# Optimization experiments

Measured on AMD Instinct MI355X. Metric: run time of the kernel, lower is better.

The kernel has to match this reference:

```python
import jax, jax.numpy as jnp
import numpy as np

STATE_DIM = 256
LATENT_DIM = 64
HIDDEN = 64
NUM_EMB = 2048
BATCH = 32768


def setup_inputs() -> dict:
    key = jax.random.key(0)
    ks = jax.random.split(key, 10)
    s = lambda *sh: 1.0 / np.sqrt(sh[0])
    return {
        "x": jax.random.normal(ks[0], (BATCH, STATE_DIM), dtype=jnp.float32),
        # encoder: Linear(state_dim, 64) -> ReLU -> Linear(64, latent_dim)
        "enc_w1": jax.random.uniform(ks[1], (STATE_DIM, HIDDEN), jnp.float32, -s(STATE_DIM), s(STATE_DIM)),
        "enc_b1": jax.random.uniform(ks[2], (HIDDEN,), jnp.float32, -s(STATE_DIM), s(STATE_DIM)),
        "enc_w2": jax.random.uniform(ks[3], (HIDDEN, LATENT_DIM), jnp.float32, -s(HIDDEN), s(HIDDEN)),
        "enc_b2": jax.random.uniform(ks[4], (LATENT_DIM,), jnp.float32, -s(HIDDEN), s(HIDDEN)),
        # codebook
        "emb": jax.random.normal(ks[5], (NUM_EMB, LATENT_DIM), dtype=jnp.float32),
        # decoder: Linear(latent_dim, 64) -> ReLU -> Linear(64, state_dim)
        "dec_w1": jax.random.uniform(ks[6], (LATENT_DIM, HIDDEN), jnp.float32, -s(LATENT_DIM), s(LATENT_DIM)),
        "dec_b1": jax.random.uniform(ks[7], (HIDDEN,), jnp.float32, -s(LATENT_DIM), s(LATENT_DIM)),
        "dec_w2": jax.random.uniform(ks[8], (HIDDEN, STATE_DIM), jnp.float32, -s(HIDDEN), s(HIDDEN)),
        "dec_b2": jax.random.uniform(ks[9], (STATE_DIM,), jnp.float32, -s(HIDDEN), s(HIDDEN)),
    }


def reference(x, enc_w1, enc_b1, enc_w2, enc_b2, emb, dec_w1, dec_b1, dec_w2, dec_b2):
    # encoder MLP: z_e [B, latent]
    h = jax.nn.relu(x @ enc_w1 + enc_b1)
    z_e = h @ enc_w2 + enc_b2
    # squared euclidean distances to codebook, expanded form: [B, K]
    # ||z - e||^2 = ||z||^2 - 2 z.e + ||e||^2  (same argmin as broadcast form)
    d = (jnp.sum(z_e * z_e, axis=1, keepdims=True)
         - 2.0 * (z_e @ emb.T)
         + jnp.sum(emb * emb, axis=1)[None, :])
    z_q_idx = jnp.argmin(d, axis=1)           # [B]
    z_q = emb[z_q_idx]                        # [B, latent]
    # decoder MLP
    hd = jax.nn.relu(z_q @ dec_w1 + dec_b1)
    x_recon = hd @ dec_w2 + dec_b2
    return (x_recon, z_e, z_q)
```

## Files before the change

### kernel.cpp

```cpp
#include <hip/hip_runtime.h>

#define BATCH   32768
#define SD      256
#define LD      64
#define HDIM    64
#define NEMB    2048
#define REFINE_THR_Q 5e-4f

typedef short  short8 __attribute__((ext_vector_type(8)));
typedef float  f32x4  __attribute__((ext_vector_type(4)));

__device__ __forceinline__ unsigned short f2bf(float f) {
    unsigned int u = __float_as_uint(f);
    u = (u + 0x7FFFu + ((u >> 16) & 1u)) >> 16;
    return (unsigned short)u;
}
__device__ __forceinline__ float bf2f(unsigned short h) {
    return __uint_as_float(((unsigned int)h) << 16);
}

__global__ __launch_bounds__(256) void k0_prep(const float* __restrict__ emb,
                                               float* __restrict__ e2q,
                                               unsigned short* __restrict__ eh,
                                               unsigned short* __restrict__ el,
                                               int* __restrict__ count) {
    int k = blockIdx.x * 256 + threadIdx.x;
    if (k == 0) *count = 0;
    const float* er = emb + (size_t)k * LD;
    unsigned short hrow[LD], lrow[LD];
    float s = 0.f;
#pragma unroll
    for (int q = 0; q < LD; ++q) {
        float v = er[q];
        s += v * v;
        unsigned short h = f2bf(v);
        hrow[q] = h;
        lrow[q] = f2bf(v - bf2f(h));
    }
    e2q[k] = -0.5f * s;
    short8* dh = (short8*)(eh + (size_t)k * LD);
    short8* dl = (short8*)(el + (size_t)k * LD);
#pragma unroll
    for (int q = 0; q < 8; ++q) {
        dh[q] = *(short8*)&hrow[q * 8];
        dl[q] = *(short8*)&lrow[q * 8];
    }
}

__global__ __launch_bounds__(256) void k0b_wsplit(const float* __restrict__ w1,
                                                  const float* __restrict__ w2,
                                                  unsigned short* __restrict__ w1h,
                                                  unsigned short* __restrict__ w1l,
                                                  unsigned short* __restrict__ w2h,
                                                  unsigned short* __restrict__ w2l) {
    int b = blockIdx.x;
    int t = threadIdx.x;
    if (b < 16) {
        int e = b * 256 + t;
        int j = e >> 6, k = e & 63;
        float v = w1[k * HDIM + j];
        unsigned short h = f2bf(v);
        w1h[e] = h; w1l[e] = f2bf(v - bf2f(h));
    } else {
        int e = (b - 16) * 256 + t;
        int j = e >> 6, k = e & 63;
        float v = w2[k * SD + j];
        unsigned short h = f2bf(v);
        w2h[e] = h; w2l[e] = f2bf(v - bf2f(h));
    }
}

__global__ __launch_bounds__(512, 4) void k_enc(const float* __restrict__ x,
                                                const float* __restrict__ w1,
                                                const float* __restrict__ b1,
                                                const float* __restrict__ w2,
                                                const float* __restrict__ b2,
                                                float* __restrict__ zOut,
                                                unsigned short* __restrict__ zh,
                                                unsigned short* __restrict__ zl) {
    __shared__ float smem[20480];
    float* w1s = smem;
    float* xs  = smem + 16384;
    int tid = threadIdx.x;
    {
        const float4* src = (const float4*)w1;
        float4* dst = (float4*)w1s;
#pragma unroll
        for (int t = 0; t < 8; ++t) dst[tid + 512 * t] = src[tid + 512 * t];
    }
    int r0 = blockIdx.x * 64;
    int sr = tid >> 3;
    int sq = tid & 7;
    const float* xrow = x + (size_t)(r0 + sr) * SD + sq * 4;
    *(float4*)&xs[sr * 32 + sq * 4] = *(const float4*)xrow;
    __syncthreads();

    int lane = tid & 63;
    int w = tid >> 6;
    float acc[8];
#pragma unroll
    for (int r = 0; r < 8; ++r) acc[r] = 0.f;

    for (int c = 0; c < 8; ++c) {
        float4 nv;
        if (c < 7) nv = *(const float4*)(xrow + (c + 1) * 32);
        const float* xb = &xs[(c & 1) * 2048 + (w * 8) * 32];
        int kb = c * 32;
#pragma unroll
        for (int i0 = 0; i0 < 32; i0 += 8) {
            float wf[8];
#pragma unroll
            for (int jj = 0; jj < 8; ++jj) wf[jj] = w1s[(kb + i0 + jj) * HDIM + lane];
#pragma unroll
            for (int r = 0; r < 8; ++r) {
                const float* xr = xb + r * 32 + i0;
                float4 xa = *(const float4*)xr;
                float4 xc = *(const float4*)(xr + 4);
                acc[r] += xa.x * wf[0] + xa.y * wf[1] + xa.z * wf[2] + xa.w * wf[3]
                        + xc.x * wf[4] + xc.y * wf[5] + xc.z * wf[6] + xc.w * wf[7];
            }
        }
        __syncthreads();
        if (c < 7) *(float4*)&xs[((c + 1) & 1) * 2048 + sr * 32 + sq * 4] = nv;
        __syncthreads();
    }

    float* hs  = smem;
    float* w2s = smem + 4096;
    float bb1 = b1[lane];
#pragma unroll
    for (int r = 0; r < 8; ++r)
        hs[(w * 8 + r) * 64 + lane] = fmaxf(acc[r] + bb1, 0.f);
    {
        const float4* src = (const float4*)w2;
        float4* dst = (float4*)w2s;
        dst[tid] = src[tid];
        dst[tid + 512] = src[tid + 512];
    }
    __syncthreads();

    const float* hb = &hs[(w * 8) * 64];
    float ac2[8];
#pragma unroll
    for (int r = 0; r < 8; ++r) ac2[r] = 0.f;

    for (int j0 = 0; j0 < HDIM; j0 += 8) {
        float wf[8];
#pragma unroll
        for (int jj = 0; jj < 8; ++jj) wf[jj] = w2s[(j0 + jj) * LD + lane];
#pragma unroll
        for (int r = 0; r < 8; ++r) {
            const float* hr = hb + r * 64 + j0;
            float4 ha = *(const float4*)hr;
            float4 hc = *(const float4*)(hr + 4);
            ac2[r] += ha.x * wf[0] + ha.y * wf[1] + ha.z * wf[2] + ha.w * wf[3]
                    + hc.x * wf[4] + hc.y * wf[5] + hc.z * wf[6] + hc.w * wf[7];
        }
    }
    float bb2 = b2[lane];
#pragma unroll
    for (int r = 0; r < 8; ++r) {
        float z = ac2[r] + bb2;
        size_t o = (size_t)(r0 + w * 8 + r) * LD + lane;
        zOut[o] = z;
        unsigned short h = f2bf(z);
        zh[o] = h;
        zl[o] = f2bf(z - bf2f(h));
    }
}

#define K2_LOAD(P, t) do {                                                  \
    const unsigned short* ph_ = ehp + (size_t)(t) * 16 * LD;                \
    const unsigned short* pl_ = elp + (size_t)(t) * 16 * LD;                \
    P##a0 = *(const short8*)(ph_);                                          \
    P##a1 = *(const short8*)(ph_ + 32);                                     \
    P##a2 = *(const short8*)(pl_);                                          \
    P##a3 = *(const short8*)(pl_ + 32);                                     \
    P##e2 = *(const f32x4*)(e2q + cbase + (t) * 16 + hi * 4);               \
} while (0)

#define K2_COMP(P, t) do {                                                  \
    f32x4 acc_[4];                                                          \
    _Pragma("unroll")                                                       \
    for (int g = 0; g < 4; ++g) {                                           \
        f32x4 c_;                                                           \
        c_ = __builtin_amdgcn_mfma_f32_16x16x32_bf16(P##a0, bh[g][0], P##e2, 0, 0, 0); \
        c_ = __builtin_amdgcn_mfma_f32_16x16x32_bf16(P##a1, bh[g][1], c_, 0, 0, 0);    \
        c_ = __builtin_amdgcn_mfma_f32_16x16x32_bf16(P##a2, bh[g][0], c_, 0, 0, 0);    \
        c_ = __builtin_amdgcn_mfma_f32_16x16x32_bf16(P##a3, bh[g][1], c_, 0, 0, 0);    \
        c_ = __builtin_amdgcn_mfma_f32_16x16x32_bf16(P##a0, bl[g][0], c_, 0, 0, 0);    \
        c_ = __builtin_amdgcn_mfma_f32_16x16x32_bf16(P##a1, bl[g][1], c_, 0, 0, 0);    \
        acc_[g] = c_;                                                       \
    }                                                                       \
    _Pragma("unroll")                                                       \
    for (int g = 0; g < 4; ++g) {                                           \
        float m_ = fmaxf(fmaxf(acc_[g][0], acc_[g][1]),                     \
                         fmaxf(acc_[g][2], acc_[g][3]));                    \
        bool win_ = (m_ > bb[g]);                                           \
        qv[g] = win_ ? acc_[g] : qv[g];                                     \
        tt[g] = win_ ? (t) : tt[g];                                         \
        b2v[g] = fmaxf(b2v[g], fminf(bb[g], m_));                           \
        bb[g] = fmaxf(bb[g], m_);                                           \
    }                                                                       \
} while (0)

__global__ __launch_bounds__(256, 2) void k2_mfma(const unsigned short* __restrict__ zh,
                                                  const unsigned short* __restrict__ zl,
                                                  const unsigned short* __restrict__ eh,
                                                  const unsigned short* __restrict__ el,
                                                  const float* __restrict__ e2q,
                                                  int* __restrict__ idx,
                                                  int* __restrict__ list,
                                                  int* __restrict__ count) {
    int tid  = threadIdx.x;
    int lane = tid & 63;
    int w    = tid >> 6;
    int rb   = blockIdx.x * 64;
    int lo   = lane & 15;
    int hi   = lane >> 4;

    short8 bh[4][2], bl[4][2];
#pragma unroll
    for (int g = 0; g < 4; ++g) {
        size_t zo = (size_t)(rb + g * 16 + lo) * LD + hi * 8;
        bh[g][0] = *(const short8*)(zh + zo);
        bh[g][1] = *(const short8*)(zh + zo + 32);
        bl[g][0] = *(const short8*)(zl + zo);
        bl[g][1] = *(const short8*)(zl + zo + 32);
    }

    float bb[4], b2v[4];
    f32x4 qv[4];
    int   tt[4];
#pragma unroll
    for (int g = 0; g < 4; ++g) {
        bb[g] = -3.0e38f; b2v[g] = -3.0e38f; tt[g] = 0;
        qv[g][0] = qv[g][1] = qv[g][2] = qv[g][3] = -3.0e38f;
    }

    const int cbase = w * (NEMB / 4);
    const unsigned short* ehp = eh + (size_t)(cbase + lo) * LD + hi * 8;
    const unsigned short* elp = el + (size_t)(cbase + lo) * LD + hi * 8;

    short8 Aa0, Aa1, Aa2, Aa3; f32x4 Ae2;
    short8 Ba0, Ba1, Ba2, Ba3; f32x4 Be2;
    short8 Ca0, Ca1, Ca2, Ca3; f32x4 Ce2;

    K2_LOAD(A, 0);
    K2_LOAD(B, 1);
    K2_LOAD(C, 2);

    for (int tb = 0; tb < 27; tb += 3) {
        K2_COMP(A, tb);     K2_LOAD(A, tb + 3);
        K2_COMP(B, tb + 1); K2_LOAD(B, tb + 4);
        K2_COMP(C, tb + 2); K2_LOAD(C, tb + 5);
    }
    K2_COMP(A, 27); K2_LOAD(A, 30);
    K2_COMP(B, 28); K2_LOAD(B, 31);
    K2_COMP(C, 29);
    K2_COMP(A, 30);
    K2_COMP(B, 31);

    float ss[4];
    int   ii[4];
#pragma unroll
    for (int g = 0; g < 4; ++g) {
        float s0 = qv[g][0], s1 = qv[g][1], s2 = qv[g][2], s3 = qv[g][3];
        float M01 = fmaxf(s0, s1), L01 = fminf(s0, s1);
        float M23 = fmaxf(s2, s3), L23 = fminf(s2, s3);
        int   d01 = (s1 > s0) ? 1 : 0;
        int   d23 = (s3 > s2) ? 3 : 2;
        bool  cp  = (M23 > M01);
        float within2 = fmaxf(fminf(M01, M23), cp ? L23 : L01);
        int   dd  = cp ? d23 : d01;
        ii[g] = cbase + tt[g] * 16 + hi * 4 + dd;
        ss[g] = fmaxf(b2v[g], within2);
    }

#pragma unroll
    for (int off = 16; off <= 32; off <<= 1) {
#pragma unroll
        for (int g = 0; g < 4; ++g) {
            float ob = __shfl_xor(bb[g], off);
            float os = __shfl_xor(ss[g], off);
            int   oi = __shfl_xor(ii[g], off);
            ss[g] = fmaxf(fmaxf(fminf(bb[g], ob), os), ss[g]);
            ii[g] = (ob > bb[g]) ? oi : ii[g];
            bb[g] = fmaxf(bb[g], ob);
        }
    }

    __shared__ float Lb[4][64];
    __shared__ float Ls[4][64];
    __shared__ int   Li[4][64];
    if (lane < 16) {
#pragma unroll
        for (int g = 0; g < 4; ++g) {
            Lb[w][g * 16 + lane] = bb[g];
            Ls[w][g * 16 + lane] = ss[g];
            Li[w][g * 16 + lane] = ii[g];
        }
    }
    __syncthreads();

    if (tid < 64) {
        float B = Lb[0][tid], S = Ls[0][tid];
        int   I = Li[0][tid];
#pragma unroll
        for (int w2 = 1; w2 < 4; ++w2) {
            float ob = Lb[w2][tid], os = Ls[w2][tid];
            int   oi = Li[w2][tid];
            S = fmaxf(fmaxf(fminf(B, ob), os), S);
            I = (ob > B) ? oi : I;
            B = fmaxf(B, ob);
        }
        idx[rb + tid] = I;
        if (B - S < REFINE_THR_Q) {
            int p = atomicAdd(count, 1);
            list[p] = rb + tid;
        }
    }
}

__global__ __launch_bounds__(256) void k3_refine(const float* __restrict__ z,
                                                 const float* __restrict__ emb,
                                                 const int* __restrict__ count,
                                                 const int* __restrict__ list,
                                                 int* __restrict__ idx) {
    __shared__ double sv[256];
    __shared__ int    sx[256];
    int tid = threadIdx.x;
    int n = *count;
    for (int g = blockIdx.x; g < n; g += gridDim.x) {
        int row = list[g];
        const float4* zr4 = (const float4*)(z + (size_t)row * LD);
        float4 zv[16];
#pragma unroll
        for (int q = 0; q < 16; ++q) zv[q] = zr4[q];

        double best = 1.0e300;
        int bi = NEMB;
#pragma unroll 2
        for (int c = 0; c < 8; ++c) {
            int k = tid * 8 + c;
            const float4* er = (const float4*)(emb + (size_t)k * LD);
            double d0 = 0.0, d1 = 0.0, d2 = 0.0, d3 = 0.0;
#pragma unroll
            for (int q = 0; q < 16; ++q) {
                float4 e4 = er[q];
                double tx = (double)zv[q].x - (double)e4.x;
                double ty = (double)zv[q].y - (double)e4.y;
                double tz = (double)zv[q].z - (double)e4.z;
                double tw = (double)zv[q].w - (double)e4.w;
                d0 += tx * tx; d1 += ty * ty; d2 += tz * tz; d3 += tw * tw;
            }
            double d = (d0 + d1) + (d2 + d3);
            if (d < best) { best = d; bi = k; }
        }
        sv[tid] = best; sx[tid] = bi;
        __syncthreads();
        for (int s = 128; s > 0; s >>= 1) {
            if (tid < s) {
                if (sv[tid + s] < sv[tid] ||
                    (sv[tid + s] == sv[tid] && sx[tid + s] < sx[tid])) {
                    sv[tid] = sv[tid + s]; sx[tid] = sx[tid + s];
                }
            }
            __syncthreads();
        }
        if (tid == 0) idx[row] = sx[0];
        __syncthreads();
    }
}

__global__ __launch_bounds__(256, 2) void k_dec(const int* __restrict__ idx,
                                                const float* __restrict__ emb,
                                                const unsigned short* __restrict__ w1h,
                                                const unsigned short* __restrict__ w1l,
                                                const float* __restrict__ b1,
                                                const unsigned short* __restrict__ w2h,
                                                const unsigned short* __restrict__ w2l,
                                                const float* __restrict__ b2,
                                                float* __restrict__ xrec,
                                                float* __restrict__ zq) {
    __shared__ float hds[4][16 * 68];
    int tid  = threadIdx.x;
    int lane = tid & 63;
    int w    = tid >> 6;
    int lo   = lane & 15;
    int hi   = lane >> 4;
    int rb   = blockIdx.x * 64 + w * 16;
    int row  = rb + lo;
    int ix   = idx[row];

    short8 zah[2], zal[2];
    {
        const float* er  = emb + (size_t)ix * LD + hi * 8;
        float* zqr = zq + (size_t)row * LD + hi * 8;
#pragma unroll
        for (int kt = 0; kt < 2; ++kt) {
            float4 a = *(const float4*)(er + kt * 32);
            float4 b = *(const float4*)(er + kt * 32 + 4);
            *(float4*)(zqr + kt * 32) = a;
            *(float4*)(zqr + kt * 32 + 4) = b;
            float v[8] = {a.x, a.y, a.z, a.w, b.x, b.y, b.z, b.w};
            unsigned short hh[8], ll[8];
#pragma unroll
            for (int q = 0; q < 8; ++q) {
                unsigned short hb = f2bf(v[q]);
                hh[q] = hb;
                ll[q] = f2bf(v[q] - bf2f(hb));
            }
            zah[kt] = *(short8*)hh;
            zal[kt] = *(short8*)ll;
        }
    }

#pragma unroll
    for (int jt = 0; jt < 4; ++jt) {
        float bj = b1[jt * 16 + lo];
        f32x4 c = {bj, bj, bj, bj};
#pragma unroll
        for (int kt = 0; kt < 2; ++kt) {
            short8 bh8 = *(const short8*)(w1h + (jt * 16 + lo) * LD + kt * 32 + hi * 8);
            short8 bl8 = *(const short8*)(w1l + (jt * 16 + lo) * LD + kt * 32 + hi * 8);
            c = __builtin_amdgcn_mfma_f32_16x16x32_bf16(zah[kt], bh8, c, 0, 0, 0);
            c = __builtin_amdgcn_mfma_f32_16x16x32_bf16(zah[kt], bl8, c, 0, 0, 0);
            c = __builtin_amdgcn_mfma_f32_16x16x32_bf16(zal[kt], bh8, c, 0, 0, 0);
        }
#pragma unroll
        for (int r = 0; r < 4; ++r)
            hds[w][(hi * 4 + r) * 68 + jt * 16 + lo] = fmaxf(c[r], 0.f);
    }
    __syncthreads();

    short8 hah[2], hal[2];
#pragma unroll
    for (int kt = 0; kt < 2; ++kt) {
        float4 a = *(const float4*)&hds[w][lo * 68 + kt * 32 + hi * 8];
        float4 b = *(const float4*)&hds[w][lo * 68 + kt * 32 + hi * 8 + 4];
        float v[8] = {a.x, a.y, a.z, a.w, b.x, b.y, b.z, b.w};
        unsigned short hh[8], ll[8];
#pragma unroll
        for (int q = 0; q < 8; ++q) {
            unsigned short hb = f2bf(v[q]);
            hh[q] = hb;
            ll[q] = f2bf(v[q] - bf2f(hb));
        }
        hah[kt] = *(short8*)hh;
        hal[kt] = *(short8*)ll;
    }

    for (int jt = 0; jt < 16; ++jt) {
        float bj = b2[jt * 16 + lo];
        f32x4 c = {bj, bj, bj, bj};
#pragma unroll
        for (int kt = 0; kt < 2; ++kt) {
            short8 bh8 = *(const short8*)(w2h + (jt * 16 + lo) * LD + kt * 32 + hi * 8);
            short8 bl8 = *(const short8*)(w2l + (jt * 16 + lo) * LD + kt * 32 + hi * 8);
            c = __builtin_amdgcn_mfma_f32_16x16x32_bf16(hah[kt], bh8, c, 0, 0, 0);
            c = __builtin_amdgcn_mfma_f32_16x16x32_bf16(hah[kt], bl8, c, 0, 0, 0);
            c = __builtin_amdgcn_mfma_f32_16x16x32_bf16(hal[kt], bh8, c, 0, 0, 0);
        }
#pragma unroll
        for (int r = 0; r < 4; ++r)
            xrec[(size_t)(rb + hi * 4 + r) * SD + jt * 16 + lo] = c[r];
    }
}

extern "C" void kernel_launch(void* const* d_in, const int* in_sizes, int n_in,
                              void* d_out, int out_size, void* d_ws, size_t ws_size,
                              hipStream_t stream) {
    const float* x   = (const float*)d_in[0];
    const float* ew1 = (const float*)d_in[1];
    const float* eb1 = (const float*)d_in[2];
    const float* ew2 = (const float*)d_in[3];
    const float* eb2 = (const float*)d_in[4];
    const float* emb = (const float*)d_in[5];
    const float* dw1 = (const float*)d_in[6];
    const float* db1 = (const float*)d_in[7];
    const float* dw2 = (const float*)d_in[8];
    const float* db2 = (const float*)d_in[9];

    float* out  = (float*)d_out;
    float* xrec = out;
    float* zE   = out + (size_t)BATCH * SD;
    float* zQ   = zE + (size_t)BATCH * LD;

    char* xb = (char*)xrec;
    unsigned short* zh  = (unsigned short*)xb;
    unsigned short* zl  = (unsigned short*)(xb + (4u << 20));
    unsigned short* eh  = (unsigned short*)(xb + (8u << 20));
    unsigned short* el  = (unsigned short*)(xb + (8u << 20) + (NEMB * LD * 2));
    float*          e2q = (float*)(xb + (9u << 20));

    char* ws = (char*)d_ws;
    int*  count = (int*)ws;
    int*  idxA  = (int*)(ws + 16384);
    int*  list  = (int*)(ws + 147456);
    unsigned short* w1h = (unsigned short*)(ws + 278528);
    unsigned short* w1l = (unsigned short*)(ws + 286720);
    unsigned short* w2h = (unsigned short*)(ws + 294912);
    unsigned short* w2l = (unsigned short*)(ws + 327680);

    hipLaunchKernelGGL(k0_prep,    dim3(NEMB / 256), dim3(256), 0, stream, emb, e2q, eh, el, count);
    hipLaunchKernelGGL(k0b_wsplit, dim3(80),         dim3(256), 0, stream, dw1, dw2, w1h, w1l, w2h, w2l);
    hipLaunchKernelGGL(k_enc,      dim3(BATCH / 64), dim3(512), 0, stream, x, ew1, eb1, ew2, eb2, zE, zh, zl);
    hipLaunchKernelGGL(k2_mfma,    dim3(BATCH / 64), dim3(256), 0, stream, zh, zl, eh, el, e2q, idxA, list, count);
    hipLaunchKernelGGL(k3_refine,  dim3(128),        dim3(256), 0, stream, zE, emb, count, list, idxA);
    hipLaunchKernelGGL(k_dec,      dim3(BATCH / 64), dim3(256), 0, stream, idxA, emb, w1h, w1l, db1, w2h, w2l, db2, xrec, zQ);
}
```

Measured before the change: 129.9 us.

## Rework encoder GEMMs as 8x8 register-tiled split-K with shared-memory reduction

The encoder kernel now stages the whole 64x256 x tile transposed in LDS. Each thread computes an 8x8 output tile with outer-product FMAs, and each of the 8 waves handles a K-slice. Partial sums are combined by a tree reduction through shared memory, and the same scheme is applied to the second layer. The goal is more FMAs per LDS load. The cost is extra syncs, a serial reduction tail done by one wave, larger LDS use (128KB) and launch bounds lowered to 2 blocks per SM.

Result: no change. 132.3 us (+1.9%).

```diff
diff --git a/kernel.cpp b/kernel.cpp
--- a/kernel.cpp
+++ b/kernel.cpp
@@ -70,7 +70,46 @@
     }
 }
 
-__global__ __launch_bounds__(512, 4) void k_enc(const float* __restrict__ x,
+__device__ __forceinline__ void wr_slice(float* red, int s, float (&a)[8][8],
+                                         int rg, int cg) {
+#pragma unroll
+    for (int cc = 0; cc < 8; ++cc) {
+        float4 v0 = {a[0][cc], a[1][cc], a[2][cc], a[3][cc]};
+        float4 v1 = {a[4][cc], a[5][cc], a[6][cc], a[7][cc]};
+        float* p = red + s * 4096 + (cg * 8 + cc) * 64 + rg * 8;
+        *(float4*)p = v0;
+        *(float4*)(p + 4) = v1;
+    }
+}
+__device__ __forceinline__ void add_slice(float* red, int s, float (&a)[8][8],
+                                          int rg, int cg) {
+#pragma unroll
+    for (int cc = 0; cc < 8; ++cc) {
+        const float* p = red + s * 4096 + (cg * 8 + cc) * 64 + rg * 8;
+        float4 v0 = *(const float4*)p;
+        float4 v1 = *(const float4*)(p + 4);
+        a[0][cc] += v0.x; a[1][cc] += v0.y; a[2][cc] += v0.z; a[3][cc] += v0.w;
+        a[4][cc] += v1.x; a[5][cc] += v1.y; a[6][cc] += v1.z; a[7][cc] += v1.w;
+    }
+}
+__device__ __forceinline__ void enc_merge(float* red, float (&a)[8][8],
+                                          int w, int rg, int cg) {
+    if (w & 1) wr_slice(red, w >> 1, a, rg, cg);
+    __syncthreads();
+    if (!(w & 1)) add_slice(red, w >> 1, a, rg, cg);
+    __syncthreads();
+    if (w == 2) wr_slice(red, 0, a, rg, cg);
+    if (w == 6) wr_slice(red, 1, a, rg, cg);
+    __syncthreads();
+    if (w == 0) add_slice(red, 0, a, rg, cg);
+    if (w == 4) add_slice(red, 1, a, rg, cg);
+    __syncthreads();
+    if (w == 4) wr_slice(red, 0, a, rg, cg);
+    __syncthreads();
+    if (w == 0) add_slice(red, 0, a, rg, cg);
+}
+
+__global__ __launch_bounds__(512, 2) void k_enc(const float* __restrict__ x,
                                                 const float* __restrict__ w1,
                                                 const float* __restrict__ b1,
                                                 const float* __restrict__ w2,
@@ -78,94 +117,139 @@
                                                 float* __restrict__ zOut,
                                                 unsigned short* __restrict__ zh,
                                                 unsigned short* __restrict__ zl) {
-    __shared__ float smem[20480];
-    float* w1s = smem;
-    float* xs  = smem + 16384;
-    int tid = threadIdx.x;
+    __shared__ float smem[32768];
+    float* xT  = smem;
+    float* w1s = smem + 16384;
+    float* red = smem;
+    float* w2s = smem + 16384;
+    float* hs  = smem + 20480;
+
+    int tid  = threadIdx.x;
+    int lane = tid & 63;
+    int w    = tid >> 6;
+    int rg   = lane & 7;
+    int cg   = lane >> 3;
+    int r0   = blockIdx.x * 64;
+
     {
+        int r = tid >> 3, kq = tid & 7;
+        const float* xr = x + (size_t)(r0 + r) * SD;
+#pragma unroll
+        for (int p = 0; p < 8; ++p) {
+            int k = p * 32 + kq * 4;
+            float4 v = *(const float4*)(xr + k);
+            xT[(k + 0) * 64 + r] = v.x;
+            xT[(k + 1) * 64 + r] = v.y;
+            xT[(k + 2) * 64 + r] = v.z;
+            xT[(k + 3) * 64 + r] = v.w;
+        }
         const float4* src = (const float4*)w1;
         float4* dst = (float4*)w1s;
 #pragma unroll
         for (int t = 0; t < 8; ++t) dst[tid + 512 * t] = src[tid + 512 * t];
     }
-    int r0 = blockIdx.x * 64;
-    int sr = tid >> 3;
-    int sq = tid & 7;
-    const float* xrow = x + (size_t)(r0 + sr) * SD + sq * 4;
-    *(float4*)&xs[sr * 32 + sq * 4] = *(const float4*)xrow;
-    __syncthreads();
-
-    int lane = tid & 63;
-    int w = tid >> 6;
-    float acc[8];
-#pragma unroll
-    for (int r = 0; r < 8; ++r) acc[r] = 0.f;
-
-    for (int c = 0; c < 8; ++c) {
-        float4 nv;
-        if (c < 7) nv = *(const float4*)(xrow + (c + 1) * 32);
-        const float* xb = &xs[(c & 1) * 2048 + (w * 8) * 32];
-        int kb = c * 32;
-#pragma unroll
-        for (int i0 = 0; i0 < 32; i0 += 8) {
-            float wf[8];
-#pragma unroll
-            for (int jj = 0; jj < 8; ++jj) wf[jj] = w1s[(kb + i0 + jj) * HDIM + lane];
-#pragma unroll
-            for (int r = 0; r < 8; ++r) {
-                const float* xr = xb + r * 32 + i0;
-                float4 xa = *(const float4*)xr;
-                float4 xc = *(const float4*)(xr + 4);
-                acc[r] += xa.x * wf[0] + xa.y * wf[1] + xa.z * wf[2] + xa.w * wf[3]
-                        + xc.x * wf[4] + xc.y * wf[5] + xc.z * wf[6] + xc.w * wf[7];
-            }
-        }
-        __syncthreads();
-        if (c < 7) *(float4*)&xs[((c + 1) & 1) * 2048 + sr * 32 + sq * 4] = nv;
-        __syncthreads();
-    }
-
-    float* hs  = smem;
-    float* w2s = smem + 4096;
-    float bb1 = b1[lane];
-#pragma unroll
-    for (int r = 0; r < 8; ++r)
-        hs[(w * 8 + r) * 64 + lane] = fmaxf(acc[r] + bb1, 0.f);
+    __syncthreads();
+
+    float acc[8][8];
+#pragma unroll
+    for (int i = 0; i < 8; ++i)
+#pragma unroll
+        for (int j = 0; j < 8; ++j) acc[i][j] = 0.f;
+    {
+        int k0 = w * 32;
+#pragma unroll 4
+        for (int k = k0; k < k0 + 32; ++k) {
+            float4 xa = *(const float4*)&xT[k * 64 + rg * 8];
+            float4 xb = *(const float4*)&xT[k * 64 + rg * 8 + 4];
+            float4 wa = *(const float4*)&w1s[k * 64 + cg * 8];
+            float4 wb = *(const float4*)&w1s[k * 64 + cg * 8 + 4];
+            float xf[8] = {xa.x, xa.y, xa.z, xa.w, xb.x, xb.y, xb.z, xb.w};
+            float wf[8] = {wa.x, wa.y, wa.z, wa.w, wb.x, wb.y, wb.z, wb.w};
+#pragma unroll
+            for (int rr = 0; rr < 8; ++rr)
+#pragma unroll
+                for (int cc = 0; cc < 8; ++cc)
+                    acc[rr][cc] = fmaf(xf[rr], wf[cc], acc[rr][cc]);
+        }
+    }
+    __syncthreads();
+
     {
         const float4* src = (const float4*)w2;
         float4* dst = (float4*)w2s;
         dst[tid] = src[tid];
         dst[tid + 512] = src[tid + 512];
     }
-    __syncthreads();
-
-    const float* hb = &hs[(w * 8) * 64];
-    float ac2[8];
-#pragma unroll
-    for (int r = 0; r < 8; ++r) ac2[r] = 0.f;
-
-    for (int j0 = 0; j0 < HDIM; j0 += 8) {
-        float wf[8];
-#pragma unroll
-        for (int jj = 0; jj < 8; ++jj) wf[jj] = w2s[(j0 + jj) * LD + lane];
-#pragma unroll
-        for (int r = 0; r < 8; ++r) {
-            const float* hr = hb + r * 64 + j0;
-            float4 ha = *(const float4*)hr;
-            float4 hc = *(const float4*)(hr + 4);
-            ac2[r] += ha.x * wf[0] + ha.y * wf[1] + ha.z * wf[2] + ha.w * wf[3]
-                    + hc.x * wf[4] + hc.y * wf[5] + hc.z * wf[6] + hc.w * wf[7];
-        }
-    }
-    float bb2 = b2[lane];
-#pragma unroll
-    for (int r = 0; r < 8; ++r) {
-        float z = ac2[r] + bb2;
-        size_t o = (size_t)(r0 + w * 8 + r) * LD + lane;
-        zOut[o] = z;
-        unsigned short h = f2bf(z);
-        zh[o] = h;
-        zl[o] = f2bf(z - bf2f(h));
+    enc_merge(red, acc, w, rg, cg);
+
+    if (w == 0) {
+        float b1v[8];
+        *(float4*)&b1v[0] = *(const float4*)(b1 + cg * 8);
+        *(float4*)&b1v[4] = *(const float4*)(b1 + cg * 8 + 4);
+#pragma unroll
+        for (int cc = 0; cc < 8; ++cc) {
+            int j = cg * 8 + cc;
+            float4 h0 = {fmaxf(acc[0][cc] + b1v[cc], 0.f),
+                         fmaxf(acc[1][cc] + b1v[cc], 0.f),
+                         fmaxf(acc[2][cc] + b1v[cc], 0.f),
+                         fmaxf(acc[3][cc] + b1v[cc], 0.f)};
+            float4 h1 = {fmaxf(acc[4][cc] + b1v[cc], 0.f),
+                         fmaxf(acc[5][cc] + b1v[cc], 0.f),
+                         fmaxf(acc[6][cc] + b1v[cc], 0.f),
+                         fmaxf(acc[7][cc] + b1v[cc], 0.f)};
+            *(float4*)&hs[j * 66 + rg * 8] = h0;
+            *(float4*)&hs[j * 66 + rg * 8 + 4] = h1;
+        }
+    }
+    __syncthreads();
+
+    float ac2[8][8];
+#pragma unroll
+    for (int i = 0; i < 8; ++i)
+#pragma unroll
+        for (int j = 0; j < 8; ++j) ac2[i][j] = 0.f;
+    {
+        int q0 = w * 8;
+#pragma unroll
+        for (int k2 = q0; k2 < q0 + 8; ++k2) {
+            float4 xa = *(const float4*)&hs[k2 * 66 + rg * 8];
+            float4 xb = *(const float4*)&hs[k2 * 66 + rg * 8 + 4];
+            float4 wa = *(const float4*)&w2s[k2 * 64 + cg * 8];
+            float4 wb = *(const float4*)&w2s[k2 * 64 + cg * 8 + 4];
+            float xf[8] = {xa.x, xa.y, xa.z, xa.w, xb.x, xb.y, xb.z, xb.w};
+            float wf[8] = {wa.x, wa.y, wa.z, wa.w, wb.x, wb.y, wb.z, wb.w};
+#pragma unroll
+            for (int rr = 0; rr < 8; ++rr)
+#pragma unroll
+                for (int cc = 0; cc < 8; ++cc)
+                    ac2[rr][cc] = fmaf(xf[rr], wf[cc], ac2[rr][cc]);
+        }
+    }
+    __syncthreads();
+    enc_merge(red, ac2, w, rg, cg);
+
+    if (w == 0) {
+        float b2v[8];
+        *(float4*)&b2v[0] = *(const float4*)(b2 + cg * 8);
+        *(float4*)&b2v[4] = *(const float4*)(b2 + cg * 8 + 4);
+#pragma unroll
+        for (int rr = 0; rr < 8; ++rr) {
+            int i = rg * 8 + rr;
+            size_t base = (size_t)(r0 + i) * LD + cg * 8;
+            float zv[8];
+            unsigned short hh[8], ll[8];
+#pragma unroll
+            for (int cc = 0; cc < 8; ++cc) {
+                zv[cc] = ac2[rr][cc] + b2v[cc];
+                unsigned short hb = f2bf(zv[cc]);
+                hh[cc] = hb;
+                ll[cc] = f2bf(zv[cc] - bf2f(hb));
+            }
+            *(float4*)(zOut + base) = *(const float4*)&zv[0];
+            *(float4*)(zOut + base + 4) = *(const float4*)&zv[4];
+            *(short8*)(zh + base) = *(const short8*)hh;
+            *(short8*)(zl + base) = *(const short8*)ll;
+        }
     }
 }
 
```
